# Optimization experiments

Measured on AMD Instinct MI355X. Metric: run time of the kernel, lower is better.

Reference implementation:

```python
import jax, jax.numpy as jnp
import numpy as np

K, N, F_IN, F_HID, F_OUT = 4, 8192, 128, 64, 16
DROPOUT_P = 0.3


def setup_inputs() -> dict:
    key = jax.random.key(0)
    ks = jax.random.split(key, 8)
    return {
        "adj": jax.random.uniform(ks[0], (K, N, N), dtype=jnp.float32),
        "x": jax.random.normal(ks[1], (N, F_IN), dtype=jnp.float32),
        "W1": jax.random.normal(ks[2], (F_IN, F_HID), dtype=jnp.float32) * 0.05,
        "b1": jax.random.normal(ks[3], (F_HID,), dtype=jnp.float32) * 0.05,
        "W2": jax.random.normal(ks[4], (F_HID, F_OUT), dtype=jnp.float32) * 0.05,
        "b2": jax.random.normal(ks[5], (F_OUT,), dtype=jnp.float32) * 0.05,
        "pi1": jax.random.normal(ks[6], (K,), dtype=jnp.float32),
        "pi2": jax.random.normal(ks[7], (K,), dtype=jnp.float32),
    }


def _gconv(adj, x, W, b, pi):
    # mixed adjacency: [N, N] = sum_k pi[k] * adj[k]
    A = jnp.einsum('k,knm->nm', pi, adj)
    support = x @ W                     # [N, F_out]
    return A @ support + b              # [N, F_out]


def reference(adj, x, W1, b1, W2, b2, pi1, pi2):
    # gc1.pi is softmax-normalized in Co_GCN.forward
    pi1_n = jax.nn.softmax(pi1)
    h = jax.nn.relu(_gconv(adj, x, W1, b1, pi1_n))   # [N, F_HID]
    # F.dropout with p=0.3, training=True (functional default): fixed-key mask
    keep = jax.random.bernoulli(jax.random.key(42), 1.0 - DROPOUT_P, h.shape)
    h = jnp.where(keep, h / (1.0 - DROPOUT_P), 0.0)
    out = _gconv(adj, h, W2, b2, pi2)                # [N, F_OUT]
    return out
```

## Files before the change

kernel.cpp:

```cpp
#include <hip/hip_runtime.h>
#include <stdint.h>

#define NN 8192
#define FIN 128
#define FH 64
#define FO 16
#define BM 64
#define BN 64
#define SPLIT1 4
#define NRANGE1 (NN / SPLIT1)
#define NCHUNK1 (NRANGE1 / BN)
#define SPLIT2 16
#define NRANGE2 (NN / SPLIT2)

typedef float    f32x4 __attribute__((ext_vector_type(4)));
typedef _Float16 f16x4 __attribute__((ext_vector_type(4)));
typedef _Float16 f16x8 __attribute__((ext_vector_type(8)));
typedef _Float16 h2    __attribute__((ext_vector_type(2)));

union U8 { f16x8 v; h2 p[4]; };

static __device__ __forceinline__ void fma4(float4& acc, float a, const float4 s) {
  acc.x = fmaf(a, s.x, acc.x);
  acc.y = fmaf(a, s.y, acc.y);
  acc.z = fmaf(a, s.z, acc.z);
  acc.w = fmaf(a, s.w, acc.w);
}

static __device__ __forceinline__ float dot2(h2 a, h2 b, float c) {
#if defined(__has_builtin)
#if __has_builtin(__builtin_amdgcn_fdot2)
  return __builtin_amdgcn_fdot2(a, b, c, false);
#else
  return c + (float)a.x * (float)b.x + (float)a.y * (float)b.y;
#endif
#else
  return c + (float)a.x * (float)b.x + (float)a.y * (float)b.y;
#endif
}

__global__ __launch_bounds__(256) void k_s1(const float* __restrict__ x,
                                            const float* __restrict__ W1,
                                            float* __restrict__ S1) {
  __shared__ float W1l[FIN * FH];
  __shared__ float xl[16][FIN + 4];
  const int t = threadIdx.x;
  const int n0 = blockIdx.x * 16;
  for (int i = t; i < FIN * FH / 4; i += 256)
    ((float4*)W1l)[i] = ((const float4*)W1)[i];
  for (int i = t; i < 16 * FIN; i += 256) {
    int r = i >> 7, c = i & (FIN - 1);
    xl[r][c] = x[(size_t)(n0 + r) * FIN + c];
  }
  __syncthreads();
  const int m = t >> 4;
  const int j0 = (t & 15) << 2;
  float4 acc = {0.f, 0.f, 0.f, 0.f};
#pragma unroll 8
  for (int k = 0; k < FIN; ++k) {
    float xv = xl[m][k];
    float4 w = *(const float4*)&W1l[k * FH + j0];
    fma4(acc, xv, w);
  }
  *(float4*)&S1[(size_t)(n0 + m) * FH + j0] = acc;
}

__global__ __launch_bounds__(256) void k_pass1_fused(const float* __restrict__ adj,
                                                     const float* __restrict__ S1,
                                                     const float* __restrict__ pi1,
                                                     const float* __restrict__ pi2,
                                                     float* __restrict__ hpart,
                                                     _Float16* __restrict__ A2h) {
  __shared__ float Alds[BN][BM];
  __shared__ float S1l[BN][FH];
  const int t = threadIdx.x;
  const int mb = blockIdx.x >> 2;
  const int sp = blockIdx.x & 3;

  float p0 = pi1[0], p1 = pi1[1], p2 = pi1[2], p3 = pi1[3];
  float mx = fmaxf(fmaxf(p0, p1), fmaxf(p2, p3));
  float e0 = expf(p0 - mx), e1 = expf(p1 - mx), e2 = expf(p2 - mx), e3 = expf(p3 - mx);
  float inv = 1.0f / (e0 + e1 + e2 + e3);
  const float w0 = e0 * inv, w1 = e1 * inv, w2 = e2 * inv, w3 = e3 * inv;
  const float v0 = pi2[0], v1 = pi2[1], v2 = pi2[2], v3 = pi2[3];

  const size_t NN2 = (size_t)NN * NN;
  const size_t row0 = (size_t)mb * BM;
  const int nbase = sp * NRANGE1;

  const int n4 = t & 15;
  const int ms = t >> 4;
  const int m0 = (t & 15) << 2;
  const int j0 = (t >> 4) << 2;

  f32x4 pf[4][4];
  f32x4 pfS[4];

  float4 acc0 = {0,0,0,0}, acc1 = {0,0,0,0}, acc2 = {0,0,0,0}, acc3 = {0,0,0,0};

  auto ISSUE = [&](int c) {
    const int n0 = nbase + c * BN;
#pragma unroll
    for (int p = 0; p < 4; ++p) {
      const float* g = adj + (row0 + (size_t)(ms + (p << 4))) * NN + (size_t)(n0 + (n4 << 2));
      pf[p][0] = __builtin_nontemporal_load((const f32x4*)g);
      pf[p][1] = __builtin_nontemporal_load((const f32x4*)(g + NN2));
      pf[p][2] = __builtin_nontemporal_load((const f32x4*)(g + 2 * NN2));
      pf[p][3] = __builtin_nontemporal_load((const f32x4*)(g + 3 * NN2));
    }
    const f32x4* src = (const f32x4*)(S1 + (size_t)n0 * FH);
#pragma unroll
    for (int i = 0; i < 4; ++i) pfS[i] = src[t + 256 * i];
  };

  auto STAGE = [&](int c) {
    const int n0 = nbase + c * BN;
#pragma unroll
    for (int p = 0; p < 4; ++p) {
      const int ml = ms + (p << 4);
      const int mc = ml ^ (n4 << 2);
      f32x4 a0 = pf[p][0], a1 = pf[p][1], a2 = pf[p][2], a3 = pf[p][3];
      Alds[(n4 << 2) + 0][mc] = fmaf(w0, a0.x, fmaf(w1, a1.x, fmaf(w2, a2.x, w3 * a3.x)));
      Alds[(n4 << 2) + 1][mc] = fmaf(w0, a0.y, fmaf(w1, a1.y, fmaf(w2, a2.y, w3 * a3.y)));
      Alds[(n4 << 2) + 2][mc] = fmaf(w0, a0.z, fmaf(w1, a1.z, fmaf(w2, a2.z, w3 * a3.z)));
      Alds[(n4 << 2) + 3][mc] = fmaf(w0, a0.w, fmaf(w1, a1.w, fmaf(w2, a2.w, w3 * a3.w)));
      f16x4 h4;
      h4.x = (_Float16)fmaf(v0, a0.x, fmaf(v1, a1.x, fmaf(v2, a2.x, v3 * a3.x)));
      h4.y = (_Float16)fmaf(v0, a0.y, fmaf(v1, a1.y, fmaf(v2, a2.y, v3 * a3.y)));
      h4.z = (_Float16)fmaf(v0, a0.z, fmaf(v1, a1.z, fmaf(v2, a2.z, v3 * a3.z)));
      h4.w = (_Float16)fmaf(v0, a0.w, fmaf(v1, a1.w, fmaf(v2, a2.w, v3 * a3.w)));
      *(f16x4*)(A2h + (row0 + (size_t)ml) * NN + (size_t)(n0 + (n4 << 2))) = h4;
    }
    f32x4* dst = (f32x4*)&S1l[0][0];
#pragma unroll
    for (int i = 0; i < 4; ++i) dst[t + 256 * i] = pfS[i];
  };

  ISSUE(0);
  for (int c = 0; c < NCHUNK1; ++c) {
    __syncthreads();
    STAGE(c);
    if (c + 1 < NCHUNK1) ISSUE(c + 1);
    asm volatile("s_waitcnt lgkmcnt(0)" ::: "memory");
    __builtin_amdgcn_s_barrier();
#pragma unroll 4
    for (int n = 0; n < BN; ++n) {
      const float4 a = *(const float4*)&Alds[n][m0 ^ (n & 60)];
      const float4 s = *(const float4*)&S1l[n][j0];
      fma4(acc0, a.x, s);
      fma4(acc1, a.y, s);
      fma4(acc2, a.z, s);
      fma4(acc3, a.w, s);
    }
  }
  float* hp = hpart + (size_t)sp * NN * FH;
  const size_t rbase = (row0 + m0) * FH + j0;
  *(float4*)&hp[rbase]          = acc0;
  *(float4*)&hp[rbase + FH]     = acc1;
  *(float4*)&hp[rbase + 2 * FH] = acc2;
  *(float4*)&hp[rbase + 3 * FH] = acc3;
}

__device__ __forceinline__ float dropout_scale(uint32_t e) {
  uint32_t x0 = 0u;
  uint32_t x1 = e;
  const uint32_t ks1 = 42u;
  const uint32_t ks2 = 0x1BD11BF0u;
  x1 += ks1;
#define TFR(d) { x0 += x1; x1 = (x1 << d) | (x1 >> (32 - d)); x1 ^= x0; }
  TFR(13) TFR(15) TFR(26) TFR(6)   x0 += ks1; x1 += ks2 + 1u;
  TFR(17) TFR(29) TFR(16) TFR(24)  x0 += ks2; x1 += 0u  + 2u;
  TFR(13) TFR(15) TFR(26) TFR(6)   x0 += 0u;  x1 += ks1 + 3u;
  TFR(17) TFR(29) TFR(16) TFR(24)  x0 += ks1; x1 += ks2 + 4u;
  TFR(13) TFR(15) TFR(26) TFR(6)   x0 += ks2; x1 += 0u  + 5u;
#undef TFR
  uint32_t bits = x0 ^ x1;
  float u = __uint_as_float((bits >> 9) | 0x3f800000u) - 1.0f;
  return (u < 0.7f) ? (1.0f / 0.7f) : 0.0f;
}

__global__ __launch_bounds__(256) void k_mid(const float* __restrict__ hpart,
                                             const float* __restrict__ b1,
                                             const float* __restrict__ W2,
                                             _Float16* __restrict__ HWT) {
  __shared__ float hl[4][FH];
  __shared__ float W2l[FH * FO];
  const int t = threadIdx.x;
  const int n0 = blockIdx.x << 2;
  for (int i = t; i < FH * FO; i += 256) W2l[i] = W2[i];
  const int j = t & 63, r = t >> 6;
  const uint32_t idx = (uint32_t)(n0 + r) * FH + j;
  const size_t NF = (size_t)NN * FH;
  float pre = b1[j];
#pragma unroll
  for (int s = 0; s < SPLIT1; ++s) pre += hpart[idx + (size_t)s * NF];
  float v = fmaxf(pre, 0.0f) * dropout_scale(idx);
  hl[r][j] = v;
  __syncthreads();
  if (t < 64) {
    const int rr = t >> 4, f = t & 15;
    float s = 0.f;
#pragma unroll 8
    for (int jj = 0; jj < FH; ++jj)
      s = fmaf(hl[rr][jj], W2l[jj * FO + f], s);
    HWT[(size_t)f * NN + (n0 + rr)] = (_Float16)s;
  }
}

__global__ __launch_bounds__(256) void k_init(const float* __restrict__ b2,
                                              float* __restrict__ out) {
  const int e = blockIdx.x * 256 + threadIdx.x;
  out[e] = b2[e & 15];
}

__global__ __launch_bounds__(64) void k_pass2_dot(const _Float16* __restrict__ A2h,
                                                  const _Float16* __restrict__ HWT,
                                                  float* __restrict__ out) {
  __shared__ f16x8 Htl[64 * 16];
  const int t = threadIdx.x;
  const int mb = blockIdx.x >> 4;
  const int sp = blockIdx.x & 15;
  const size_t row0 = (size_t)mb * BM;
  const int nbase = sp * NRANGE2;

#pragma unroll
  for (int i = 0; i < FO; ++i)
    Htl[t * FO + i] = *(const f16x8*)(HWT + (size_t)i * NN + nbase + t * 8);
  __syncthreads();

  const int fgrp = t & 3;
  const int mgrp = t >> 2;
  const size_t rbase = (row0 + (size_t)mgrp * 4) * NN + nbase;

  float acc[4][4];
#pragma unroll
  for (int j = 0; j < 4; ++j)
#pragma unroll
    for (int i = 0; i < 4; ++i) acc[j][i] = 0.f;

  f16x8 aA[4], aB[4];
#pragma unroll
  for (int j = 0; j < 4; ++j)
    aA[j] = *(const f16x8*)(A2h + rbase + (size_t)j * NN);

  auto LOADB = [&](int o) {
#pragma unroll
    for (int j = 0; j < 4; ++j)
      aB[j] = *(const f16x8*)(A2h + rbase + (size_t)j * NN + o * 8);
  };
  auto LOADA = [&](int o) {
#pragma unroll
    for (int j = 0; j < 4; ++j)
      aA[j] = *(const f16x8*)(A2h + rbase + (size_t)j * NN + o * 8);
  };

  auto COMPUTE = [&](const f16x8* buf, int o) {
    U8 h0, h1, h2v, h3;
    h0.v  = Htl[o * FO + fgrp * 4 + 0];
    h1.v  = Htl[o * FO + fgrp * 4 + 1];
    h2v.v = Htl[o * FO + fgrp * 4 + 2];
    h3.v  = Htl[o * FO + fgrp * 4 + 3];
#pragma unroll
    for (int j = 0; j < 4; ++j) {
      U8 a;
      a.v = buf[j];
#pragma unroll
      for (int q = 0; q < 4; ++q) {
        h2 pa = a.p[q];
        acc[j][0] = dot2(pa, h0.p[q],  acc[j][0]);
        acc[j][1] = dot2(pa, h1.p[q],  acc[j][1]);
        acc[j][2] = dot2(pa, h2v.p[q], acc[j][2]);
        acc[j][3] = dot2(pa, h3.p[q],  acc[j][3]);
      }
    }
  };

  for (int o = 0; o < 64; o += 2) {
    LOADB(o + 1);
    COMPUTE(aA, o);
    if (o + 2 < 64) LOADA(o + 2);
    COMPUTE(aB, o + 1);
  }

#pragma unroll
  for (int j = 0; j < 4; ++j)
#pragma unroll
    for (int i = 0; i < 4; ++i)
      atomicAdd(&out[(row0 + (size_t)mgrp * 4 + j) * FO + fgrp * 4 + i], acc[j][i]);
}

extern "C" void kernel_launch(void* const* d_in, const int* in_sizes, int n_in,
                              void* d_out, int out_size, void* d_ws, size_t ws_size,
                              hipStream_t stream) {
  const float* adj = (const float*)d_in[0];
  const float* x   = (const float*)d_in[1];
  const float* W1  = (const float*)d_in[2];
  const float* b1  = (const float*)d_in[3];
  const float* W2  = (const float*)d_in[4];
  const float* b2  = (const float*)d_in[5];
  const float* pi1 = (const float*)d_in[6];
  const float* pi2 = (const float*)d_in[7];
  float* out = (float*)d_out;
  float* ws  = (float*)d_ws;

  float* S1    = ws;
  float* hpart = S1 + (size_t)NN * FH;
  _Float16* A2h = (_Float16*)(hpart + (size_t)SPLIT1 * NN * FH);
  _Float16* HWT = A2h + (size_t)NN * NN;

  k_s1         <<<NN / 16,            256, 0, stream>>>(x, W1, S1);
  k_pass1_fused<<<(NN / BM) * SPLIT1, 256, 0, stream>>>(adj, S1, pi1, pi2, hpart, A2h);
  k_mid        <<<NN / 4,             256, 0, stream>>>(hpart, b1, W2, HWT);
  k_init       <<<(NN * FO) / 256,    256, 0, stream>>>(b2, out);
  k_pass2_dot  <<<(NN / BM) * SPLIT2,  64, 0, stream>>>(A2h, HWT, out);
}
```

Baseline: 349.2 us.

## Use fp16 packed dot2 for pass-1 adjacency-times-support inner product

The first-layer support matrix is stored in fp16, pair-interleaved along the reduction dimension, and the mixed adjacency tile is converted to fp16 pairs in LDS. The pass-1 inner loop then uses fdot2 instructions with fp32 accumulation instead of scalar fp32 FMAs. This halves LDS footprint and LDS read traffic and halves the instruction count per product. In exchange, the first-layer aggregation loses precision, and the LDS swizzle scheme changes.

```diff
diff --git a/kernel.cpp b/kernel.cpp
--- a/kernel.cpp
+++ b/kernel.cpp
@@ -41,9 +41,10 @@
 
 __global__ __launch_bounds__(256) void k_s1(const float* __restrict__ x,
                                             const float* __restrict__ W1,
-                                            float* __restrict__ S1) {
+                                            _Float16* __restrict__ S1p) {
   __shared__ float W1l[FIN * FH];
   __shared__ float xl[16][FIN + 4];
+  __shared__ float hl[16][FH];
   const int t = threadIdx.x;
   const int n0 = blockIdx.x * 16;
   for (int i = t; i < FIN * FH / 4; i += 256)
@@ -62,17 +63,28 @@
     float4 w = *(const float4*)&W1l[k * FH + j0];
     fma4(acc, xv, w);
   }
-  *(float4*)&S1[(size_t)(n0 + m) * FH + j0] = acc;
+  *(float4*)&hl[m][j0] = acc;
+  __syncthreads();
+  const int j = t & 63;
+  const int g = t >> 6;
+#pragma unroll
+  for (int e = 0; e < 2; ++e) {
+    const int np = g * 2 + e;
+    h2 v;
+    v.x = (_Float16)hl[np * 2 + 0][j];
+    v.y = (_Float16)hl[np * 2 + 1][j];
+    *(h2*)&S1p[(((size_t)(n0 >> 1) + np) * FH + j) * 2] = v;
+  }
 }
 
 __global__ __launch_bounds__(256) void k_pass1_fused(const float* __restrict__ adj,
-                                                     const float* __restrict__ S1,
+                                                     const _Float16* __restrict__ S1p,
                                                      const float* __restrict__ pi1,
                                                      const float* __restrict__ pi2,
                                                      float* __restrict__ hpart,
                                                      _Float16* __restrict__ A2h) {
-  __shared__ float Alds[BN][BM];
-  __shared__ float S1l[BN][FH];
+  __shared__ h2 Alds[BN / 2][BM];
+  __shared__ _Float16 S1l[BN / 2][FH][2];
   const int t = threadIdx.x;
   const int mb = blockIdx.x >> 2;
   const int sp = blockIdx.x & 3;
@@ -94,7 +106,7 @@
   const int j0 = (t >> 4) << 2;
 
   f32x4 pf[4][4];
-  f32x4 pfS[4];
+  f16x8 pfS[2];
 
   float4 acc0 = {0,0,0,0}, acc1 = {0,0,0,0}, acc2 = {0,0,0,0}, acc3 = {0,0,0,0};
 
@@ -108,9 +120,9 @@
       pf[p][2] = __builtin_nontemporal_load((const f32x4*)(g + 2 * NN2));
       pf[p][3] = __builtin_nontemporal_load((const f32x4*)(g + 3 * NN2));
     }
-    const f32x4* src = (const f32x4*)(S1 + (size_t)n0 * FH);
-#pragma unroll
-    for (int i = 0; i < 4; ++i) pfS[i] = src[t + 256 * i];
+    const f16x8* src = (const f16x8*)(S1p + (size_t)(n0 >> 1) * FH * 2);
+    pfS[0] = src[t];
+    pfS[1] = src[t + 256];
   };
 
   auto STAGE = [&](int c) {
@@ -118,12 +130,16 @@
 #pragma unroll
     for (int p = 0; p < 4; ++p) {
       const int ml = ms + (p << 4);
-      const int mc = ml ^ (n4 << 2);
       f32x4 a0 = pf[p][0], a1 = pf[p][1], a2 = pf[p][2], a3 = pf[p][3];
-      Alds[(n4 << 2) + 0][mc] = fmaf(w0, a0.x, fmaf(w1, a1.x, fmaf(w2, a2.x, w3 * a3.x)));
-      Alds[(n4 << 2) + 1][mc] = fmaf(w0, a0.y, fmaf(w1, a1.y, fmaf(w2, a2.y, w3 * a3.y)));
-      Alds[(n4 << 2) + 2][mc] = fmaf(w0, a0.z, fmaf(w1, a1.z, fmaf(w2, a2.z, w3 * a3.z)));
-      Alds[(n4 << 2) + 3][mc] = fmaf(w0, a0.w, fmaf(w1, a1.w, fmaf(w2, a2.w, w3 * a3.w)));
+      float c0 = fmaf(w0, a0.x, fmaf(w1, a1.x, fmaf(w2, a2.x, w3 * a3.x)));
+      float c1 = fmaf(w0, a0.y, fmaf(w1, a1.y, fmaf(w2, a2.y, w3 * a3.y)));
+      float c2 = fmaf(w0, a0.z, fmaf(w1, a1.z, fmaf(w2, a2.z, w3 * a3.z)));
+      float c3 = fmaf(w0, a0.w, fmaf(w1, a1.w, fmaf(w2, a2.w, w3 * a3.w)));
+      const int np0 = n4 * 2, np1 = np0 + 1;
+      h2 u01; u01.x = (_Float16)c0; u01.y = (_Float16)c1;
+      h2 u23; u23.x = (_Float16)c2; u23.y = (_Float16)c3;
+      Alds[np0][ml ^ ((np0 & 7) << 2)] = u01;
+      Alds[np1][ml ^ ((np1 & 7) << 2)] = u23;
       f16x4 h4;
       h4.x = (_Float16)fmaf(v0, a0.x, fmaf(v1, a1.x, fmaf(v2, a2.x, v3 * a3.x)));
       h4.y = (_Float16)fmaf(v0, a0.y, fmaf(v1, a1.y, fmaf(v2, a2.y, v3 * a3.y)));
@@ -131,9 +147,9 @@
       h4.w = (_Float16)fmaf(v0, a0.w, fmaf(v1, a1.w, fmaf(v2, a2.w, v3 * a3.w)));
       *(f16x4*)(A2h + (row0 + (size_t)ml) * NN + (size_t)(n0 + (n4 << 2))) = h4;
     }
-    f32x4* dst = (f32x4*)&S1l[0][0];
-#pragma unroll
-    for (int i = 0; i < 4; ++i) dst[t + 256 * i] = pfS[i];
+    f16x8* dst = (f16x8*)&S1l[0][0][0];
+    dst[t]       = pfS[0];
+    dst[t + 256] = pfS[1];
   };
 
   ISSUE(0);
@@ -144,13 +160,26 @@
     asm volatile("s_waitcnt lgkmcnt(0)" ::: "memory");
     __builtin_amdgcn_s_barrier();
 #pragma unroll 4
-    for (int n = 0; n < BN; ++n) {
-      const float4 a = *(const float4*)&Alds[n][m0 ^ (n & 60)];
-      const float4 s = *(const float4*)&S1l[n][j0];
-      fma4(acc0, a.x, s);
-      fma4(acc1, a.y, s);
-      fma4(acc2, a.z, s);
-      fma4(acc3, a.w, s);
+    for (int np = 0; np < BN / 2; ++np) {
+      const int s = (np & 7) << 2;
+      U8 a;  a.v  = *(const f16x8*)&Alds[np][m0 ^ s];
+      U8 sv; sv.v = *(const f16x8*)&S1l[np][j0][0];
+      acc0.x = dot2(a.p[0], sv.p[0], acc0.x);
+      acc0.y = dot2(a.p[0], sv.p[1], acc0.y);
+      acc0.z = dot2(a.p[0], sv.p[2], acc0.z);
+      acc0.w = dot2(a.p[0], sv.p[3], acc0.w);
+      acc1.x = dot2(a.p[1], sv.p[0], acc1.x);
+      acc1.y = dot2(a.p[1], sv.p[1], acc1.y);
+      acc1.z = dot2(a.p[1], sv.p[2], acc1.z);
+      acc1.w = dot2(a.p[1], sv.p[3], acc1.w);
+      acc2.x = dot2(a.p[2], sv.p[0], acc2.x);
+      acc2.y = dot2(a.p[2], sv.p[1], acc2.y);
+      acc2.z = dot2(a.p[2], sv.p[2], acc2.z);
+      acc2.w = dot2(a.p[2], sv.p[3], acc2.w);
+      acc3.x = dot2(a.p[3], sv.p[0], acc3.x);
+      acc3.y = dot2(a.p[3], sv.p[1], acc3.y);
+      acc3.z = dot2(a.p[3], sv.p[2], acc3.z);
+      acc3.w = dot2(a.p[3], sv.p[3], acc3.w);
     }
   }
   float* hp = hpart + (size_t)sp * NN * FH;
@@ -303,13 +332,13 @@
   float* out = (float*)d_out;
   float* ws  = (float*)d_ws;
 
-  float* S1    = ws;
-  float* hpart = S1 + (size_t)NN * FH;
-  _Float16* A2h = (_Float16*)(hpart + (size_t)SPLIT1 * NN * FH);
+  float* hpart  = ws;
+  _Float16* S1p = (_Float16*)(hpart + (size_t)SPLIT1 * NN * FH);
+  _Float16* A2h = S1p + (size_t)NN * FH;
   _Float16* HWT = A2h + (size_t)NN * NN;
 
-  k_s1         <<<NN / 16,            256, 0, stream>>>(x, W1, S1);
-  k_pass1_fused<<<(NN / BM) * SPLIT1, 256, 0, stream>>>(adj, S1, pi1, pi2, hpart, A2h);
+  k_s1         <<<NN / 16,            256, 0, stream>>>(x, W1, S1p);
+  k_pass1_fused<<<(NN / BM) * SPLIT1, 256, 0, stream>>>(adj, S1p, pi1, pi2, hpart, A2h);
   k_mid        <<<NN / 4,             256, 0, stream>>>(hpart, b1, W2, HWT);
   k_init       <<<(NN * FO) / 256,    256, 0, stream>>>(b2, out);
   k_pass2_dot  <<<(NN / BM) * SPLIT2,  64, 0, stream>>>(A2h, HWT, out);
```

After: 337.0 us. -3.5%, faster.
